# Kernel tuning notes

Measured on AMD Instinct MI355X. Metric: run time of the kernel, lower is better.

The kernel has to match this reference:

```python
import jax, jax.numpy as jnp
import numpy as np

# ---- static skeleton structure (SMPL 24-joint, 23-edge kinematic tree) ----
SMPL_EDGES = [[0,1],[0,2],[0,3],[1,4],[2,5],[3,6],[4,7],[5,8],[6,9],[7,10],
              [8,11],[9,12],[9,13],[9,14],[12,15],[13,16],[14,17],[16,18],
              [17,19],[18,20],[19,21],[20,22],[21,23]]
KERNEL, STRIDE, PAD, DIST = 15, 2, 7, 1

def _edge_dist(edges):
    E = len(edges)
    m = np.full((E, E), 1e6)
    np.fill_diagonal(m, 0.0)
    for i, a in enumerate(edges):
        for j, b in enumerate(edges):
            if i != j and set(a) & set(b):
                m[i, j] = 1.0
    for k in range(E):  # Floyd-Warshall on the edge adjacency graph
        m = np.minimum(m, m[:, k:k+1] + m[k:k+1, :])
    return m

def _find_neighbor(edges, d, n_global):
    m = _edge_dist(edges); E = len(edges)
    nb = [list(np.nonzero(m[i] <= d)[0]) for i in range(E)]
    gp = list(nb[0])  # edges near root edge (keeps deep-motion-editing's known quirk)
    g_ids = [E + k for k in range(n_global)]
    for i in gp:
        nb[i].extend(g_ids)
    for _ in range(n_global):
        nb.append(gp + g_ids)
    return nb

def _find_seqs(edges):
    deg = {}
    for a, b in edges:
        deg[a] = deg.get(a, 0) + 1
        deg[b] = deg.get(b, 0) + 1
    seqs = []
    def rec(j, seq):
        if deg.get(j, 0) > 2 and j != 0:
            seqs.append(seq); seq = []
        if deg.get(j, 0) == 1:
            seqs.append(seq); return
        for idx, (a, b) in enumerate(edges):
            if a == j:
                rec(b, seq + [idx])
    rec(0, [])
    return seqs

def _pooling(edges, last_pool, global_ids):
    pools, new_edges = [], []
    for seq in _find_seqs(edges):
        if last_pool:
            pools.append(seq); continue
        if len(seq) % 2 == 1:
            pools.append([seq[0]]); new_edges.append(edges[seq[0]]); seq = seq[1:]
        for i in range(0, len(seq), 2):
            pools.append([seq[i], seq[i+1]])
            new_edges.append([edges[seq[i]][0], edges[seq[i+1]][1]])
    pools.append(list(global_ids))
    return pools, new_edges

def _conv_mask(nb, in_per, out_per):
    N = len(nb)
    mask = np.zeros((N*out_per, N*in_per, 1), np.float32)
    for i, ns in enumerate(nb):
        for j in ns:
            mask[i*out_per:(i+1)*out_per, j*in_per:(j+1)*in_per, 0] = 1.0
    return mask

def _pool_matrix(pools, n_nodes, cpe):
    W = np.zeros((len(pools)*cpe, n_nodes*cpe), np.float32)
    c = np.arange(cpe)
    for i, grp in enumerate(pools):
        for j in grp:
            W[i*cpe + c, j*cpe + c] = 1.0 / len(grp)
    return W

E0 = len(SMPL_EDGES)
N0 = E0 + 2  # 23 edges + global position node + root-velocity node (the '+4' channels)
MASK0 = jnp.asarray(_conv_mask(_find_neighbor(SMPL_EDGES, DIST, 2), 4, 8))  # (200,100,1)
_pools0, EDGES1 = _pooling(SMPL_EDGES, False, [E0, E0 + 1])
P0 = jnp.asarray(_pool_matrix(_pools0, N0, 8))  # (112,200)
N1 = len(EDGES1) + 1
MASK1 = jnp.asarray(_conv_mask(_find_neighbor(EDGES1, DIST, 1), 8, 16))  # (224,112,1)
_pools1, _ = _pooling(EDGES1, True, [N1 - 1])
P1 = jnp.asarray(_pool_matrix(_pools1, N1, 16))  # (112,224)

IN0, OUT0 = 4 * N0, 8 * N0    # 100, 200
IN1, OUT1 = 8 * N1, 16 * N1   # 112, 224
B, T_IN = 64, 2047            # 2048 frames after zero-frame append


def _skel_conv(x, w, b, mask):
    # masked Conv1d (skeleton-sparse weights), stride 2, zero padding 7, k=15
    y = jax.lax.conv_general_dilated(x, w * mask, window_strides=(STRIDE,),
                                     padding=[(PAD, PAD)],
                                     dimension_numbers=('NCH', 'OIH', 'NCH'))
    return y + b[None, :, None]


def _forward(x, w0, b0, w1, b1):
    # x: (B, T, C); append one zero frame on time dim, then to (B, C, T+1)
    out = jnp.concatenate([x, jnp.zeros_like(x[:, :1, :])], axis=1)
    out = out.transpose(0, 2, 1)
    out = jax.nn.relu(jnp.einsum('pc,bct->bpt', P0, _skel_conv(out, w0, b0, MASK0)))
    out = jax.nn.relu(jnp.einsum('pc,bct->bpt', P1, _skel_conv(out, w1, b1, MASK1)))
    return out  # (B, 112, (T+1)//4)


def setup_inputs() -> dict:
    key = jax.random.key(0)
    k = jax.random.split(key, 5)
    s = 0.05
    return {
        'x':  jax.random.normal(k[0], (B, T_IN, IN0), jnp.float32),
        'w0': jax.random.normal(k[1], (OUT0, IN0, KERNEL), jnp.float32) * s,
        'b0': jax.random.normal(k[2], (OUT0,), jnp.float32) * s,
        'w1': jax.random.normal(k[3], (OUT1, IN1, KERNEL), jnp.float32) * s,
        'b1': jax.random.normal(k[4], (OUT1,), jnp.float32) * s,
    }


def reference(x, w0, b0, w1, b1):
    return _forward(x, w0, b0, w1, b1)
```

## Files before the change

### kernel.cpp

```cpp
#include <hip/hip_runtime.h>


#define OFF_A2  107520u
#define OFF_BF0 322560u
#define OFF_BF1 323008u

typedef unsigned int uint32;
typedef __attribute__((ext_vector_type(8))) short bs8;
typedef __attribute__((ext_vector_type(4))) float f32x4;
union U8 { uint4 u; bs8 s; };

__constant__ int c_pool0_len[14] = {2,2,2,2,1,2,2,1,2,2,1,2,2,2};
__constant__ int c_pool0_mem[14][2] = {{0,3},{6,9},{1,4},{7,10},{2,2},{5,8},{11,14},{12,12},
                                       {15,17},{19,21},{13,13},{16,18},{20,22},{23,24}};
__constant__ unsigned c_nbm0[25] = {
 0x180000Fu,0x1800017u,0x1800027u,0x1800049u,0x92u,0x124u,0x248u,0x490u,
 0x3920u,0x240u,0x480u,0x7900u,0xB900u,0x13900u,0x4800u,0x29000u,
 0x52000u,0xA8000u,0x150000u,0x2A0000u,0x540000u,0x280000u,0x500000u,
 0x180000Fu,0x180000Fu
};
__constant__ int c_pool1_len[7] = {2,2,2,1,3,3,1};
__constant__ int c_pool1_mem[7][3] = {{0,1,1},{2,3,3},{4,5,5},{6,6,6},{7,8,9},{10,11,12},{13,13,13}};
__constant__ unsigned c_nbm1[14] = {
 0x2017u,0x2003u,0x201Du,0xCu,0x2035u,0x4F0u,0x4E0u,0x5E0u,
 0x380u,0x300u,0xCE0u,0x1C00u,0x1800u,0x2017u
};
__constant__ int c_g1p[7][2] = {{0,13},{1,3},{2,4},{5,6},{7,10},{8,11},{9,12}};
__constant__ int c_U1[7][8] = {
 {0,1,2,3,6,23,24,25},
 {3,4,6,7,9,10,25,25},
 {0,1,2,4,5,7,23,24},
 {2,5,8,11,12,13,14,25},
 {8,11,12,13,15,16,25,25},
 {12,13,15,16,17,18,19,20},
 {17,18,19,20,21,22,25,25}};
__constant__ int c_U2[7][8] = {
 {0,1,2,4,13,14,14,14},
 {0,2,3,4,13,14,14,14},
 {0,2,4,5,6,7,10,13},
 {5,6,7,10,14,14,14,14},
 {5,6,7,8,9,10,14,14},
 {5,6,7,10,11,12,14,14},
 {0,1,2,4,13,14,14,14}};
__constant__ unsigned c_pk1a[7] = {0xC0301000u,0xC8483018u,0xB8281000u,0x70604010u,
                                   0xC8786040u,0x98887860u,0xC8A89888u};
__constant__ unsigned c_pk1b[7] = {0xC8B81808u,0xC8503820u,0xC0382008u,0xC8685828u,
                                   0xC8806858u,0xA0908068u,0xC8B0A090u};
__constant__ unsigned c_pk2[7][2] = {
 {0x40201000u,0xE0E0E0D0u},{0x40302000u,0xE0E0E0D0u},{0x50402000u,0xD0A07060u},
 {0xA0706050u,0xE0E0E0E0u},{0x80706050u,0xE0E0A090u},{0xA0706050u,0xE0E0C0B0u},
 {0x40201000u,0xE0E0E0D0u}};

__device__ __forceinline__ uint32 f2bf(float v) {
  uint32 u = __float_as_uint(v);
  return (u + 0x7fffu + ((u >> 16) & 1u)) >> 16;
}

__global__ void prep_fused_weights(const float* __restrict__ w0, const float* __restrict__ b0,
                                   const float* __restrict__ w1, const float* __restrict__ b1,
                                   char* __restrict__ wsb) {
  int t = blockIdx.x * blockDim.x + threadIdx.x;
  if (t < 6720) {
    int lane = t & 63;
    int r = t >> 6;
    int k = r % 15, g = r / 15;
    int m = lane & 15, h = lane >> 4;
    int pool = (m < 8) ? c_g1p[g][0] : c_g1p[g][1];
    int c = m & 7;
    int L = c_pool0_len[pool];
    float inv = 1.f / (float)L;
    uint32 us[8];
#pragma unroll
    for (int j = 0; j < 8; ++j) {
      int node = c_U1[g][2 * h + (j >> 2)];
      int ci = j & 3;
      float v = 0.f;
      if (node < 25) {
        for (int jj = 0; jj < L; ++jj) {
          int mem = c_pool0_mem[pool][jj];
          if ((c_nbm0[mem] >> node) & 1u)
            v += w0[(mem * 8 + c) * 1500 + (node * 4 + ci) * 15 + k];
        }
        v *= inv;
      }
      us[j] = f2bf(v);
    }
    uint4 o = make_uint4(us[0] | (us[1] << 16), us[2] | (us[3] << 16),
                         us[4] | (us[5] << 16), us[6] | (us[7] << 16));
    reinterpret_cast<uint4*>(wsb)[t] = o;
  } else if (t < 6720 + 13440) {
    int t2 = t - 6720;
    int lane = t2 & 63;
    int r = t2 >> 6;
    int k = r % 15;
    int r2 = r / 15;
    int ks = r2 & 1, p = r2 >> 1;
    int c = lane & 15, h = lane >> 4;
    int node = c_U2[p][ks * 4 + h];
    int L = c_pool1_len[p];
    float inv = 1.f / (float)L;
    uint32 us[8];
#pragma unroll
    for (int j = 0; j < 8; ++j) {
      float v = 0.f;
      if (node < 14) {
        for (int jj = 0; jj < L; ++jj) {
          int mem = c_pool1_mem[p][jj];
          if ((c_nbm1[mem] >> node) & 1u)
            v += w1[(mem * 16 + c) * 1680 + (node * 8 + j) * 15 + k];
        }
        v *= inv;
      }
      us[j] = f2bf(v);
    }
    uint4 o = make_uint4(us[0] | (us[1] << 16), us[2] | (us[3] << 16),
                         us[4] | (us[5] << 16), us[6] | (us[7] << 16));
    reinterpret_cast<uint4*>(wsb + OFF_A2)[t2] = o;
  } else if (t < 6720 + 13440 + 112) {
    int p = t - (6720 + 13440);
    int i = p >> 3, c = p & 7;
    int L = c_pool0_len[i];
    float v = 0.f;
    for (int jj = 0; jj < L; ++jj) v += b0[c_pool0_mem[i][jj] * 8 + c];
    reinterpret_cast<float*>(wsb + OFF_BF0)[p] = v / (float)L;
  } else if (t < 6720 + 13440 + 224) {
    int p = t - (6720 + 13440 + 112);
    int i = p >> 4, c = p & 15;
    int L = c_pool1_len[i];
    float v = 0.f;
    for (int jj = 0; jj < L; ++jj) v += b1[c_pool1_mem[i][jj] * 16 + c];
    reinterpret_cast<float*>(wsb + OFF_BF1)[p] = v / (float)L;
  }
}

__global__ __launch_bounds__(448, 4) void conv_fused(const float* __restrict__ x,
                                                     const char* __restrict__ wsb,
                                                     float* __restrict__ out) {
  __shared__ __align__(16) unsigned char xs[109 * 256];
  __shared__ __align__(16) unsigned char ys[48 * 256];
  float* const ysf = reinterpret_cast<float*>(ys);
  const int tid = threadIdx.x;
  const int lane = tid & 63;
  const int g = tid >> 6;
  const int m16 = lane & 15, h = lane >> 4;
  const int b = blockIdx.y;
  const int t0 = blockIdx.x << 4;
  const int f0y = 2 * t0 - 7;
  const int g0x = 4 * t0 - 21;
  const float* __restrict__ xb = x + (size_t)b * (2047 * 100);

  float4 rg[7];
#pragma unroll
  for (int i = 0; i < 7; ++i) {
    rg[i] = make_float4(0.f, 0.f, 0.f, 0.f);
    int e = tid + i * 448;
    if (e < 2725) {
      int f = e / 25, q = e - f * 25;
      int gt = g0x + f;
      if ((unsigned)gt < 2047u)
        rg[i] = *reinterpret_cast<const float4*>(xb + gt * 100 + 4 * q);
    }
  }
  for (int e = tid; e < 109; e += 448)
    *reinterpret_cast<uint2*>(xs + e * 256 + (200u ^ (((e >> 1) & 15) << 3))) =
        make_uint2(0u, 0u);
#pragma unroll
  for (int i = 0; i < 7; ++i) {
    int e = tid + i * 448;
    if (e < 2725) {
      int f = e / 25, q = e - f * 25;
      uint2 w = make_uint2(f2bf(rg[i].x) | (f2bf(rg[i].y) << 16),
                           f2bf(rg[i].z) | (f2bf(rg[i].w) << 16));
      *reinterpret_cast<uint2*>(xs + f * 256 + ((q * 8) ^ (((f >> 1) & 15) << 3))) = w;
    }
  }
  const uint4* __restrict__ A1p = reinterpret_cast<const uint4*>(wsb) + g * 960 + lane;
  U8 aw[15];
#pragma unroll
  for (int k = 0; k < 15; ++k) aw[k].u = A1p[k * 64];
  const int pa = c_g1p[g][0], pb = c_g1p[g][1];
  const int chbase = (h < 2) ? (pa * 8 + 4 * h) : (pb * 8 + 4 * (h - 2));
  const float4 bv0 = *reinterpret_cast<const float4*>(wsb + OFF_BF0 + chbase * 4);
  __syncthreads();

  const uint32 offA = (c_pk1a[g] >> (8 * h)) & 255u;
  const uint32 offB = (c_pk1b[g] >> (8 * h)) & 255u;
  f32x4 acc1[3];
#pragma unroll
  for (int nt = 0; nt < 3; ++nt) acc1[nt] = (f32x4)0.f;
#pragma unroll
  for (int k = 0; k < 15; ++k) {
    const uint32 sw = (uint32)(((m16 + (k >> 1)) & 15) << 3);
    const uint32 a0 = offA ^ sw, a1o = offB ^ sw;
    const unsigned char* base = xs + (2 * m16 + k) * 256;
#pragma unroll
    for (int nt = 0; nt < 3; ++nt) {
      uint2 lo = *reinterpret_cast<const uint2*>(base + nt * 8192 + a0);
      uint2 hi = *reinterpret_cast<const uint2*>(base + nt * 8192 + a1o);
      U8 bfr; bfr.u = make_uint4(lo.x, lo.y, hi.x, hi.y);
      acc1[nt] = __builtin_amdgcn_mfma_f32_16x16x32_bf16(aw[k].s, bfr.s, acc1[nt], 0, 0, 0);
    }
  }

  const uint4* __restrict__ A2p =
      reinterpret_cast<const uint4*>(wsb + OFF_A2) + g * 1920 + lane;
#pragma unroll
  for (int k = 0; k < 15; ++k) aw[k].u = A2p[k * 64];
  const float4 bv1 = *reinterpret_cast<const float4*>(wsb + OFF_BF1 + (g * 16 + 4 * h) * 4);

#pragma unroll
  for (int nt = 0; nt < 3; ++nt) {
    int row = nt * 16 + m16;
    int fy = f0y + row;
    float o0 = fmaxf(acc1[nt][0] + bv0.x, 0.f);
    float o1 = fmaxf(acc1[nt][1] + bv0.y, 0.f);
    float o2 = fmaxf(acc1[nt][2] + bv0.z, 0.f);
    float o3 = fmaxf(acc1[nt][3] + bv0.w, 0.f);
    uint2 wpk = make_uint2(f2bf(o0) | (f2bf(o1) << 16), f2bf(o2) | (f2bf(o3) << 16));
    if ((unsigned)fy >= 1024u) wpk = make_uint2(0u, 0u);
    *reinterpret_cast<uint2*>(ys + row * 256 +
        (((uint32)(chbase * 2)) ^ (((row >> 1) & 7) << 4))) = wpk;
  }
  for (int e = tid; e < 48; e += 448)
    *reinterpret_cast<uint4*>(ys + e * 256 + (224u ^ (((e >> 1) & 7) << 4))) =
        make_uint4(0u, 0u, 0u, 0u);
  __syncthreads();

  f32x4 acc2 = (f32x4)0.f;
  {
    const uint32 noff = (c_pk2[g][0] >> (8 * h)) & 255u;
#pragma unroll
    for (int k = 0; k < 15; ++k) {
      const uint32 sw = (uint32)(((m16 + (k >> 1)) & 7) << 4);
      U8 bf;
      bf.u = *reinterpret_cast<const uint4*>(ys + (2 * m16 + k) * 256 + (noff ^ sw));
      acc2 = __builtin_amdgcn_mfma_f32_16x16x32_bf16(aw[k].s, bf.s, acc2, 0, 0, 0);
    }
  }
#pragma unroll
  for (int k = 0; k < 15; ++k) aw[k].u = A2p[(15 + k) * 64];
  {
    const uint32 noff = (c_pk2[g][1] >> (8 * h)) & 255u;
#pragma unroll
    for (int k = 0; k < 15; ++k) {
      const uint32 sw = (uint32)(((m16 + (k >> 1)) & 7) << 4);
      U8 bf;
      bf.u = *reinterpret_cast<const uint4*>(ys + (2 * m16 + k) * 256 + (noff ^ sw));
      acc2 = __builtin_amdgcn_mfma_f32_16x16x32_bf16(aw[k].s, bf.s, acc2, 0, 0, 0);
    }
  }
  __syncthreads();

  {
    int t = m16;
    ysf[(g * 16 + 4 * h + 0) * 20 + t] = fmaxf(acc2[0] + bv1.x, 0.f);
    ysf[(g * 16 + 4 * h + 1) * 20 + t] = fmaxf(acc2[1] + bv1.y, 0.f);
    ysf[(g * 16 + 4 * h + 2) * 20 + t] = fmaxf(acc2[2] + bv1.z, 0.f);
    ysf[(g * 16 + 4 * h + 3) * 20 + t] = fmaxf(acc2[3] + bv1.w, 0.f);
  }
  __syncthreads();
  {
    int ch = tid >> 2, jj = tid & 3;
    float4 v = *reinterpret_cast<const float4*>(ysf + ch * 20 + jj * 4);
    *reinterpret_cast<float4*>(out + ((size_t)b * 112 + ch) * 512 + t0 + jj * 4) = v;
  }
}

extern "C" void kernel_launch(void* const* d_in, const int* in_sizes, int n_in,
                              void* d_out, int out_size, void* d_ws, size_t ws_size,
                              hipStream_t stream) {
  const float* x  = (const float*)d_in[0];
  const float* w0 = (const float*)d_in[1];
  const float* b0 = (const float*)d_in[2];
  const float* w1 = (const float*)d_in[3];
  const float* b1 = (const float*)d_in[4];
  char* wsb = (char*)d_ws;
  float* out = (float*)d_out;

  prep_fused_weights<<<80, 256, 0, stream>>>(w0, b0, w1, b1, wsb);
  conv_fused<<<dim3(32, 64), 448, 0, stream>>>(x, wsb, out);
}
```

Before: 61.97 us.

## Double per-block time tile to 32 with 14 waves sharing the input halo

Each block now covers 32 output frames with 896 threads. Two groups of seven waves split the first convolution's time tiles (3 and 2) and each computes 16 output frames of the second convolution. The input and intermediate buffers now share one LDS region, which needs an extra barrier before the overwrite. The final output is written straight from registers as scalar stores instead of being staged through LDS. This cuts the redundant halo loads and first-conv recompute per output frame and removes two barriers, but halves the grid to 1024 blocks, raises per-block LDS, and makes the global stores less coalesced.

```diff
diff --git a/kernel.cpp b/kernel.cpp
--- a/kernel.cpp
+++ b/kernel.cpp
@@ -133,45 +133,47 @@
   }
 }
 
-__global__ __launch_bounds__(448, 4) void conv_fused(const float* __restrict__ x,
+__global__ __launch_bounds__(896, 4) void conv_fused(const float* __restrict__ x,
                                                      const char* __restrict__ wsb,
                                                      float* __restrict__ out) {
-  __shared__ __align__(16) unsigned char xs[109 * 256];
-  __shared__ __align__(16) unsigned char ys[48 * 256];
-  float* const ysf = reinterpret_cast<float*>(ys);
+  __shared__ __align__(16) unsigned char lds[173 * 256];
+  unsigned char* const xs = lds;
+  unsigned char* const ys = lds;
   const int tid = threadIdx.x;
   const int lane = tid & 63;
-  const int g = tid >> 6;
+  const int w = tid >> 6;
+  const int g = (w < 7) ? w : (w - 7);
+  const int half = (w < 7) ? 0 : 1;
   const int m16 = lane & 15, h = lane >> 4;
   const int b = blockIdx.y;
-  const int t0 = blockIdx.x << 4;
+  const int t0 = blockIdx.x << 5;
   const int f0y = 2 * t0 - 7;
   const int g0x = 4 * t0 - 21;
+
   const float* __restrict__ xb = x + (size_t)b * (2047 * 100);
-
-  float4 rg[7];
-#pragma unroll
-  for (int i = 0; i < 7; ++i) {
+  float4 rg[5];
+#pragma unroll
+  for (int i = 0; i < 5; ++i) {
     rg[i] = make_float4(0.f, 0.f, 0.f, 0.f);
-    int e = tid + i * 448;
-    if (e < 2725) {
+    int e = tid + i * 896;
+    if (e < 4325) {
       int f = e / 25, q = e - f * 25;
       int gt = g0x + f;
       if ((unsigned)gt < 2047u)
         rg[i] = *reinterpret_cast<const float4*>(xb + gt * 100 + 4 * q);
     }
   }
-  for (int e = tid; e < 109; e += 448)
+  for (int e = tid; e < 173; e += 896)
     *reinterpret_cast<uint2*>(xs + e * 256 + (200u ^ (((e >> 1) & 15) << 3))) =
         make_uint2(0u, 0u);
 #pragma unroll
-  for (int i = 0; i < 7; ++i) {
-    int e = tid + i * 448;
-    if (e < 2725) {
+  for (int i = 0; i < 5; ++i) {
+    int e = tid + i * 896;
+    if (e < 4325) {
       int f = e / 25, q = e - f * 25;
-      uint2 w = make_uint2(f2bf(rg[i].x) | (f2bf(rg[i].y) << 16),
-                           f2bf(rg[i].z) | (f2bf(rg[i].w) << 16));
-      *reinterpret_cast<uint2*>(xs + f * 256 + ((q * 8) ^ (((f >> 1) & 15) << 3))) = w;
+      uint2 wv = make_uint2(f2bf(rg[i].x) | (f2bf(rg[i].y) << 16),
+                            f2bf(rg[i].z) | (f2bf(rg[i].w) << 16));
+      *reinterpret_cast<uint2*>(xs + f * 256 + ((q * 8) ^ (((f >> 1) & 15) << 3))) = wv;
     }
   }
   const uint4* __restrict__ A1p = reinterpret_cast<const uint4*>(wsb) + g * 960 + lane;
@@ -186,19 +188,34 @@
   const uint32 offA = (c_pk1a[g] >> (8 * h)) & 255u;
   const uint32 offB = (c_pk1b[g] >> (8 * h)) & 255u;
   f32x4 acc1[3];
-#pragma unroll
-  for (int nt = 0; nt < 3; ++nt) acc1[nt] = (f32x4)0.f;
-#pragma unroll
-  for (int k = 0; k < 15; ++k) {
-    const uint32 sw = (uint32)(((m16 + (k >> 1)) & 15) << 3);
-    const uint32 a0 = offA ^ sw, a1o = offB ^ sw;
-    const unsigned char* base = xs + (2 * m16 + k) * 256;
-#pragma unroll
-    for (int nt = 0; nt < 3; ++nt) {
-      uint2 lo = *reinterpret_cast<const uint2*>(base + nt * 8192 + a0);
-      uint2 hi = *reinterpret_cast<const uint2*>(base + nt * 8192 + a1o);
-      U8 bfr; bfr.u = make_uint4(lo.x, lo.y, hi.x, hi.y);
-      acc1[nt] = __builtin_amdgcn_mfma_f32_16x16x32_bf16(aw[k].s, bfr.s, acc1[nt], 0, 0, 0);
+  acc1[0] = (f32x4)0.f; acc1[1] = (f32x4)0.f; acc1[2] = (f32x4)0.f;
+  if (half == 0) {
+#pragma unroll
+    for (int k = 0; k < 15; ++k) {
+      const uint32 sw = (uint32)(((m16 + (k >> 1)) & 15) << 3);
+      const uint32 a0 = offA ^ sw, a1o = offB ^ sw;
+      const unsigned char* base = xs + (2 * m16 + k) * 256;
+#pragma unroll
+      for (int nt = 0; nt < 3; ++nt) {
+        uint2 lo = *reinterpret_cast<const uint2*>(base + nt * 8192 + a0);
+        uint2 hi = *reinterpret_cast<const uint2*>(base + nt * 8192 + a1o);
+        U8 bfr; bfr.u = make_uint4(lo.x, lo.y, hi.x, hi.y);
+        acc1[nt] = __builtin_amdgcn_mfma_f32_16x16x32_bf16(aw[k].s, bfr.s, acc1[nt], 0, 0, 0);
+      }
+    }
+  } else {
+#pragma unroll
+    for (int k = 0; k < 15; ++k) {
+      const uint32 sw = (uint32)(((m16 + (k >> 1)) & 15) << 3);
+      const uint32 a0 = offA ^ sw, a1o = offB ^ sw;
+      const unsigned char* base = xs + (2 * m16 + k) * 256 + 3 * 8192;
+#pragma unroll
+      for (int nt = 0; nt < 2; ++nt) {
+        uint2 lo = *reinterpret_cast<const uint2*>(base + nt * 8192 + a0);
+        uint2 hi = *reinterpret_cast<const uint2*>(base + nt * 8192 + a1o);
+        U8 bfr; bfr.u = make_uint4(lo.x, lo.y, hi.x, hi.y);
+        acc1[nt] = __builtin_amdgcn_mfma_f32_16x16x32_bf16(aw[k].s, bfr.s, acc1[nt], 0, 0, 0);
+      }
     }
   }
 
@@ -207,33 +224,38 @@
 #pragma unroll
   for (int k = 0; k < 15; ++k) aw[k].u = A2p[k * 64];
   const float4 bv1 = *reinterpret_cast<const float4*>(wsb + OFF_BF1 + (g * 16 + 4 * h) * 4);
-
-#pragma unroll
-  for (int nt = 0; nt < 3; ++nt) {
-    int row = nt * 16 + m16;
+  __syncthreads();
+
+  const int ntN = (half == 0) ? 3 : 2;
+  const int ntB = (half == 0) ? 0 : 3;
+#pragma unroll 3
+  for (int ntl = 0; ntl < ntN; ++ntl) {
+    int row = (ntB + ntl) * 16 + m16;
     int fy = f0y + row;
-    float o0 = fmaxf(acc1[nt][0] + bv0.x, 0.f);
-    float o1 = fmaxf(acc1[nt][1] + bv0.y, 0.f);
-    float o2 = fmaxf(acc1[nt][2] + bv0.z, 0.f);
-    float o3 = fmaxf(acc1[nt][3] + bv0.w, 0.f);
+    float o0 = fmaxf(acc1[ntl][0] + bv0.x, 0.f);
+    float o1 = fmaxf(acc1[ntl][1] + bv0.y, 0.f);
+    float o2 = fmaxf(acc1[ntl][2] + bv0.z, 0.f);
+    float o3 = fmaxf(acc1[ntl][3] + bv0.w, 0.f);
     uint2 wpk = make_uint2(f2bf(o0) | (f2bf(o1) << 16), f2bf(o2) | (f2bf(o3) << 16));
     if ((unsigned)fy >= 1024u) wpk = make_uint2(0u, 0u);
     *reinterpret_cast<uint2*>(ys + row * 256 +
         (((uint32)(chbase * 2)) ^ (((row >> 1) & 7) << 4))) = wpk;
   }
-  for (int e = tid; e < 48; e += 448)
+  for (int e = tid; e < 80; e += 896)
     *reinterpret_cast<uint4*>(ys + e * 256 + (224u ^ (((e >> 1) & 7) << 4))) =
         make_uint4(0u, 0u, 0u, 0u);
   __syncthreads();
 
   f32x4 acc2 = (f32x4)0.f;
+  const uint32 htoff = (uint32)(half * 8192);
   {
     const uint32 noff = (c_pk2[g][0] >> (8 * h)) & 255u;
 #pragma unroll
     for (int k = 0; k < 15; ++k) {
       const uint32 sw = (uint32)(((m16 + (k >> 1)) & 7) << 4);
       U8 bf;
-      bf.u = *reinterpret_cast<const uint4*>(ys + (2 * m16 + k) * 256 + (noff ^ sw));
+      bf.u = *reinterpret_cast<const uint4*>(ys + 2 * m16 * 256 + (noff ^ sw)
+                                             + k * 256 + htoff);
       acc2 = __builtin_amdgcn_mfma_f32_16x16x32_bf16(aw[k].s, bf.s, acc2, 0, 0, 0);
     }
   }
@@ -245,24 +267,18 @@
     for (int k = 0; k < 15; ++k) {
       const uint32 sw = (uint32)(((m16 + (k >> 1)) & 7) << 4);
       U8 bf;
-      bf.u = *reinterpret_cast<const uint4*>(ys + (2 * m16 + k) * 256 + (noff ^ sw));
+      bf.u = *reinterpret_cast<const uint4*>(ys + 2 * m16 * 256 + (noff ^ sw)
+                                             + k * 256 + htoff);
       acc2 = __builtin_amdgcn_mfma_f32_16x16x32_bf16(aw[k].s, bf.s, acc2, 0, 0, 0);
     }
   }
-  __syncthreads();
 
   {
-    int t = m16;
-    ysf[(g * 16 + 4 * h + 0) * 20 + t] = fmaxf(acc2[0] + bv1.x, 0.f);
-    ysf[(g * 16 + 4 * h + 1) * 20 + t] = fmaxf(acc2[1] + bv1.y, 0.f);
-    ysf[(g * 16 + 4 * h + 2) * 20 + t] = fmaxf(acc2[2] + bv1.z, 0.f);
-    ysf[(g * 16 + 4 * h + 3) * 20 + t] = fmaxf(acc2[3] + bv1.w, 0.f);
-  }
-  __syncthreads();
-  {
-    int ch = tid >> 2, jj = tid & 3;
-    float4 v = *reinterpret_cast<const float4*>(ysf + ch * 20 + jj * 4);
-    *reinterpret_cast<float4*>(out + ((size_t)b * 112 + ch) * 512 + t0 + jj * 4) = v;
+    size_t obase = ((size_t)b * 112 + g * 16 + 4 * h) * 512 + t0 + half * 16 + m16;
+    out[obase]        = fmaxf(acc2[0] + bv1.x, 0.f);
+    out[obase + 512]  = fmaxf(acc2[1] + bv1.y, 0.f);
+    out[obase + 1024] = fmaxf(acc2[2] + bv1.z, 0.f);
+    out[obase + 1536] = fmaxf(acc2[3] + bv1.w, 0.f);
   }
 }
 
@@ -278,5 +294,5 @@
   float* out = (float*)d_out;
 
   prep_fused_weights<<<80, 256, 0, stream>>>(w0, b0, w1, b1, wsb);
-  conv_fused<<<dim3(32, 64), 448, 0, stream>>>(x, wsb, out);
-}
+  conv_fused<<<dim3(16, 64), 896, 0, stream>>>(x, wsb, out);
+}
```

After: 61.49 us. About the same (-0.8%).
